# Optimization experiments

Hardware: AMD Instinct MI355X
Metric: run time of the kernel (lower is better)

Reference implementation:

```python
import jax, jax.numpy as jnp
import numpy as np

C = 64
CR = C // 8  # reduced channels for Q/K


def _conv1x1(x, W, b):
    # 1x1 conv == per-pixel linear over channels: x [b,c,h,w], W [o,c], b [o]
    return jnp.einsum('bchw,oc->bohw', x, W) + b[None, :, None, None]


def setup_inputs() -> dict:
    key = jax.random.key(0)
    ks = jax.random.split(key, 12)
    b, c, h, w = 8, C, 48, 48
    s = 1.0 / np.sqrt(c)
    inp = {
        'x1': jax.random.normal(ks[0], (b, c, h, w), jnp.float32),
        'x2': jax.random.normal(ks[1], (b, c, h, w), jnp.float32),
        'Wqk1': jax.random.normal(ks[2], (2 * CR, c), jnp.float32) * s,
        'bqk1': jnp.zeros((2 * CR,), jnp.float32),
        'Wqk2': jax.random.normal(ks[3], (2 * CR, c), jnp.float32) * s,
        'bqk2': jnp.zeros((2 * CR,), jnp.float32),
        'Wv1': jax.random.normal(ks[4], (c, c), jnp.float32) * s,
        'bv1': jnp.zeros((c,), jnp.float32),
        'Wv2': jax.random.normal(ks[5], (c, c), jnp.float32) * s,
        'bv2': jnp.zeros((c,), jnp.float32),
        'gamma': jnp.zeros((1,), jnp.float32) + 0.1,  # nonzero so output depends on attn
        'beta': jnp.zeros((1,), jnp.float32) + 0.1,
    }
    return inp


def reference(x1, x2, Wqk1, bqk1, Wqk2, bqk2, Wv1, bv1, Wv2, bv2, gamma, beta):
    b, c, h, w = x1.shape
    n = h * w
    qk1 = _conv1x1(x1, Wqk1, bqk1)
    qk2 = _conv1x1(x2, Wqk2, bqk2)
    q1, k1 = qk1[:, :CR], qk1[:, CR:]
    q2, k2 = qk2[:, :CR], qk2[:, CR:]
    # flatten spatial: [b, cr, n]
    q1 = q1.reshape(b, CR, n); k1 = k1.reshape(b, CR, n)
    q2 = q2.reshape(b, CR, n); k2 = k2.reshape(b, CR, n)
    v1 = _conv1x1(x1, Wv1, bv1).reshape(b, c, n)
    v2 = _conv1x1(x2, Wv2, bv2).reshape(b, c, n)
    # attn[b,i,j] = softmax_j( q[:, :, i] . k[:, :, j] )
    attn1 = jax.nn.softmax(jnp.einsum('bci,bcj->bij', q1, k1), axis=-1)
    attn2 = jax.nn.softmax(jnp.einsum('bci,bcj->bij', q2, k2), axis=-1)
    # out[:, :, j] = sum_i v[:, :, i] * attn[:, i, j]
    o1 = jnp.einsum('bci,bij->bcj', v1, attn2).reshape(b, c, h, w) * gamma + x1
    o2 = jnp.einsum('bci,bij->bcj', v2, attn1).reshape(b, c, h, w) * beta + x2
    return (o1, o2)
```

## Files before the change

### kernel.cpp

```cpp
#include <hip/hip_runtime.h>
#include <hip/hip_bf16.h>

#define NB   8
#define CCH  64
#define CR8  8
#define NPX  2304
#define BCN  (NB*CCH*NPX)
#define LOG2E 1.4426950408889634f

typedef short  short8   __attribute__((ext_vector_type(8)));
typedef unsigned short ushort8t __attribute__((ext_vector_type(8)));
typedef float  float4t  __attribute__((ext_vector_type(4)));
typedef float  float16t __attribute__((ext_vector_type(16)));

static __device__ __forceinline__ float fexp2(float x) {
    return __builtin_amdgcn_exp2f(x);
}
static __device__ __forceinline__ unsigned short bf16r(float f) {
    return (unsigned short)((__float_as_uint(f) + 0x8000u) >> 16);
}
static __device__ __forceinline__ unsigned int pack_bf16(float lo, float hi) {
    const unsigned int ul = __float_as_uint(lo) + 0x8000u;
    const unsigned int uh = __float_as_uint(hi) + 0x8000u;
    return __builtin_amdgcn_perm(uh, ul, 0x07060302u);
}
static __device__ __forceinline__ short8 pack8(const float* f) {
    union { unsigned int u[4]; short8 s; } r;
    #pragma unroll
    for (int j = 0; j < 4; j++) r.u[j] = pack_bf16(f[2*j], f[2*j+1]);
    return r.s;
}

#define WS_QB1 0
#define WS_KB1 (WS_QB1 + 147456)
#define WS_QB2 (WS_KB1 + 147456)
#define WS_KB2 (WS_QB2 + 147456)
#define WS_V1  (WS_KB2 + 147456)
#define WS_V2  (WS_V1 + BCN/2)
#define WS_PD  (WS_V2 + BCN/2)

__global__ __launch_bounds__(256) void proj_kernel(
    const float* __restrict__ x1, const float* __restrict__ x2,
    const float* __restrict__ Wqk1, const float* __restrict__ bqk1,
    const float* __restrict__ Wqk2, const float* __restrict__ bqk2,
    const float* __restrict__ Wv1,  const float* __restrict__ bv1,
    const float* __restrict__ Wv2,  const float* __restrict__ bv2,
    float* __restrict__ ws, float* __restrict__ out)
{
    const int t    = threadIdx.x;
    const int lane = t & 63;
    const int w    = t >> 6;
    const int n16  = lane & 15;
    const int c4   = lane >> 4;
    const int nt   = w & 1;
    const int mh   = w >> 1;
    const int b    = blockIdx.y;
    const int px   = blockIdx.x * 32 + nt * 16 + n16;

    const float* xsb[2];
    xsb[0] = x1 + ((size_t)b * CCH) * NPX + px;
    xsb[1] = x2 + ((size_t)b * CCH) * NPX + px;

    float xr[2][16];
    short8 bfrag[2][2];
    #pragma unroll
    for (int st = 0; st < 2; st++) {
        #pragma unroll
        for (int ch = 0; ch < 2; ch++) {
            #pragma unroll
            for (int j = 0; j < 8; j++)
                xr[st][ch * 8 + j] = xsb[st][(ch * 32 + c4 * 8 + j) * NPX];
            bfrag[st][ch] = pack8(&xr[st][ch * 8]);
        }
    }

    if (mh == 0) {
        #pragma unroll
        for (int st = 0; st < 2; st++) {
            float* outs = out + (st ? (size_t)BCN : 0);
            #pragma unroll
            for (int e = 0; e < 16; e++) {
                const int ch = (e >> 3) * 32 + c4 * 8 + (e & 7);
                outs[((size_t)b * CCH + ch) * NPX + px] = xr[st][e];
            }
        }
    }

    float4t acc[5];
    #pragma unroll
    for (int mt = 0; mt < 5; mt++) { acc[mt][0]=0.f; acc[mt][1]=0.f; acc[mt][2]=0.f; acc[mt][3]=0.f; }

    #pragma unroll
    for (int mt = 0; mt < 5; mt++) {
        const int mi  = mh * 5 + mt;
        const int isqk = (mi < 2);
        const int st  = isqk ? (mi & 1) : (mi >= 6);
        const float* Wb;
        int rowbase;
        if (isqk) { Wb = (mi == 0) ? Wqk1 : Wqk2; rowbase = 0; }
        else      { Wb = (mi >= 6) ? Wv2 : Wv1; rowbase = (mi - (mi >= 6 ? 6 : 2)) * 16; }
        const float* wrow = Wb + (size_t)(rowbase + n16) * 64 + c4 * 8;

        const short8 bf0 = st ? bfrag[1][0] : bfrag[0][0];
        const short8 bf1 = st ? bfrag[1][1] : bfrag[0][1];

        #pragma unroll
        for (int ch = 0; ch < 2; ch++) {
            float fa[8];
            const float4 a0 = *(const float4*)(wrow + ch * 32);
            const float4 a1 = *(const float4*)(wrow + ch * 32 + 4);
            fa[0] = a0.x; fa[1] = a0.y; fa[2] = a0.z; fa[3] = a0.w;
            fa[4] = a1.x; fa[5] = a1.y; fa[6] = a1.z; fa[7] = a1.w;
            acc[mt] = __builtin_amdgcn_mfma_f32_16x16x32_bf16(
                pack8(fa), ch ? bf1 : bf0, acc[mt], 0, 0, 0);
        }
    }

    #pragma unroll
    for (int mt = 0; mt < 5; mt++) {
        const int mi = mh * 5 + mt;
        if (mi < 2) {
            const int st = mi & 1;
            const float* bqk = st ? bqk2 : bqk1;
            unsigned short* qb = (unsigned short*)(ws + (st ? WS_QB2 : WS_QB1));
            unsigned short* kb = (unsigned short*)(ws + (st ? WS_KB2 : WS_KB1));
            const size_t rbase = (size_t)(b * NPX + px) * 16;
            #pragma unroll
            for (int r = 0; r < 4; r++) {
                const int oc = c4 * 4 + r;
                const float val = acc[mt][r] + bqk[oc];
                if (oc < 8)
                    qb[rbase + oc] = bf16r(val * LOG2E);
                else
                    kb[rbase + (oc - 8)] = bf16r(val);
            }
            ushort8t zq, zk;
            #pragma unroll
            for (int e = 0; e < 8; e++) { zq[e] = 0; zk[e] = 0; }
            zk[0] = 0x3F80; zk[1] = 0x3F80;
            if (c4 == 0) *(ushort8t*)(qb + rbase + 8) = zq;
            if (c4 == 2) *(ushort8t*)(kb + rbase + 8) = zk;
        } else {
            const int st = (mi >= 6);
            const int vt_ = mi - (st ? 6 : 2);
            const float* bv = st ? bv2 : bv1;
            unsigned short* v = (unsigned short*)(ws + (st ? WS_V2 : WS_V1));
            #pragma unroll
            for (int r = 0; r < 4; r++) {
                const int oc = vt_ * 16 + c4 * 4 + r;
                const float val = acc[mt][r] + bv[oc];
                v[((size_t)b * CCH + oc) * NPX + px] = bf16r(val);
            }
        }
    }
}

__global__ __launch_bounds__(256) void stats_kernel(float* __restrict__ ws)
{
    const int t  = threadIdx.x;
    const int w  = t >> 6;
    const int n  = t & 31;
    const int h  = (t & 63) >> 5;
    const int jsb = blockIdx.x;
    const int iq  = blockIdx.y;
    const int ab  = blockIdx.z;
    const int b   = ab & 7;
    const int a   = ab >> 3;

    const unsigned short* qb = (const unsigned short*)(ws + (a ? WS_QB2 : WS_QB1));
    const unsigned short* kb = (const unsigned short*)(ws + (a ? WS_KB2 : WS_KB1));
    float* pd = ws + WS_PD;

    __shared__ float red[4][288];

    const int j = jsb * 128 + w * 32 + n;
    const short8 kfrag = *(const short8*)(kb + (size_t)(b * NPX + j) * 16 + h * 8);

    const unsigned short* qp = qb + (size_t)(b * NPX + iq * 288 + n) * 16 + h * 8;
    short8 qf = *(const short8*)qp;

    for (int ib = 0; ib < 9; ib++) {
        qp += 512;
        short8 qn = qf;
        if (ib + 1 < 9) qn = *(const short8*)qp;
        float16t acc = {};
        acc = __builtin_amdgcn_mfma_f32_32x32x16_bf16(kfrag, qf, acc, 0, 0, 0);
        float s0 = 0.f, s1 = 0.f, s2 = 0.f, s3 = 0.f;
        #pragma unroll
        for (int r = 0; r < 4; r++) {
            s0 += fexp2(acc[4 * r + 0]);
            s1 += fexp2(acc[4 * r + 1]);
            s2 += fexp2(acc[4 * r + 2]);
            s3 += fexp2(acc[4 * r + 3]);
        }
        float ssum = (s0 + s1) + (s2 + s3);
        ssum += __shfl_xor(ssum, 32);
        if (h == 0) red[w][ib * 32 + n] = ssum;
        qf = qn;
    }
    __syncthreads();
    for (int idx = t; idx < 288; idx += 256)
        pd[((size_t)ab * 18 + jsb) * NPX + iq * 288 + idx] =
            red[0][idx] + red[1][idx] + red[2][idx] + red[3][idx];
}

__global__ __launch_bounds__(256) void merge_fold(float* __restrict__ ws)
{
    const float* pd = ws + WS_PD;
    const int t  = threadIdx.x;
    const int il = t & 63;
    const int pg = t >> 6;
    const int i  = blockIdx.x * 64 + il;
    const int ab = blockIdx.y;
    const int b  = ab & 7;
    const int a  = ab >> 3;

    __shared__ float red[4][64];

    const float* pb = pd + (size_t)ab * 18 * NPX + i;
    float d = 0.f;
    #pragma unroll
    for (int c = pg; c < 18; c += 4)
        d += pb[(size_t)c * NPX];
    red[pg][il] = d;
    __syncthreads();

    if (t < 64) {
        const float dt = (red[0][t] + red[1][t]) + (red[2][t] + red[3][t]);
        const float m = -__log2f(dt);
        const unsigned short mh = bf16r(m);
        __hip_bfloat16 hb; *(unsigned short*)&hb = mh;
        const unsigned short ml = bf16r(m - __bfloat162float(hb));
        unsigned short* qb = (unsigned short*)(ws + (a ? WS_QB2 : WS_QB1));
        const size_t rbase = (size_t)(b * NPX + blockIdx.x * 64 + t) * 16;
        qb[rbase + 8] = mh;
        qb[rbase + 9] = ml;
    }
}

__global__ __launch_bounds__(256) void out_kernel(
    const float* __restrict__ gamma, const float* __restrict__ beta,
    const float* __restrict__ ws, float* __restrict__ out)
{
    const int t  = threadIdx.x;
    const int jt = blockIdx.x;
    const int b  = blockIdx.y;
    const int z  = blockIdx.z;
    const int o  = z >> 2;
    const int ihalf = z & 3;

    const int a = o ? 0 : 1;
    const unsigned short* qb = (const unsigned short*)(ws + (a ? WS_QB2 : WS_QB1));
    const unsigned short* kb = (const unsigned short*)(ws + (a ? WS_KB2 : WS_KB1));
    const unsigned short* v  = (const unsigned short*)(ws + (o ? WS_V2 : WS_V1));
    const float  scale = o ? beta[0] : gamma[0];

    __shared__ unsigned short vt[64][72];
    __shared__ unsigned short pt[64][72];

    const int j0   = jt * 64;
    const int lane = t & 63;
    const int w    = t >> 6;
    const int n    = lane & 31;
    const int h    = lane >> 5;
    const int jh   = w & 1;
    const int ihq  = w >> 1;
    const int cbase = 32 * (w & 1);
    const int jbase = 32 * (w >> 1);

    const short8 kfrag = *(const short8*)(kb + (size_t)(b * NPX + j0 + 32 * jh + n) * 16 + h * 8);

    const int c0 = t >> 3, s80 = (t & 7) * 8;
    const int c1 = (t + 256) >> 3, s81 = ((t + 256) & 7) * 8;

    const int ibase = ihalf * 576;
    const unsigned short* vp0 = v + ((size_t)b * CCH + c0) * NPX + ibase + s80;
    const unsigned short* vp1 = v + ((size_t)b * CCH + c1) * NPX + ibase + s81;
    const unsigned short* qp  = qb + (size_t)(b * NPX + ibase + 32 * ihq + n) * 16 + h * 8;

    float4 vpre0 = *(const float4*)vp0;
    float4 vpre1 = *(const float4*)vp1;
    short8 qpre  = *(const short8*)qp;

    float16t oacc = {};

    for (int it = 0; it < 9; it++) {
        vp0 += 64; vp1 += 64; qp += 64 * 16;
        float4 vn0 = vpre0, vn1 = vpre1;
        short8 qn = qpre;
        if (it + 1 < 9) {
            vn0 = *(const float4*)vp0;
            vn1 = *(const float4*)vp1;
            qn  = *(const short8*)qp;
        }

        __syncthreads();

        *(float4*)&vt[c0][s80] = vpre0;
        *(float4*)&vt[c1][s81] = vpre1;

        float16t sc = {};
        sc = __builtin_amdgcn_mfma_f32_32x32x16_bf16(qpre, kfrag, sc, 0, 0, 0);

        #pragma unroll
        for (int gq = 0; gq < 4; gq++) {
            const int ibl = 32 * ihq + 8 * gq + 4 * h;
            uint2 pk;
            pk.x = pack_bf16(fexp2(sc[gq * 4 + 0]), fexp2(sc[gq * 4 + 1]));
            pk.y = pack_bf16(fexp2(sc[gq * 4 + 2]), fexp2(sc[gq * 4 + 3]));
            *(uint2*)&pt[32 * jh + n][ibl] = pk;
        }
        __syncthreads();

        #pragma unroll
        for (int kk = 0; kk < 4; kk++) {
            const short8 afrag = *(const short8*)&vt[cbase + n][kk * 16 + h * 8];
            const short8 bfrag = *(const short8*)&pt[jbase + n][kk * 16 + h * 8];
            oacc = __builtin_amdgcn_mfma_f32_32x32x16_bf16(afrag, bfrag, oacc, 0, 0, 0);
        }

        vpre0 = vn0; vpre1 = vn1; qpre = qn;
    }

    float* outp = out + (o ? BCN : 0) + (b * CCH + cbase) * NPX + j0 + jbase + n;
    #pragma unroll
    for (int r = 0; r < 16; r++) {
        const int row = (r & 3) + 8 * (r >> 2) + 4 * h;
        atomicAdd(outp + row * NPX, oacc[r] * scale);
    }
}

extern "C" void kernel_launch(void* const* d_in, const int* in_sizes, int n_in,
                              void* d_out, int out_size, void* d_ws, size_t ws_size,
                              hipStream_t stream)
{
    const float* x1   = (const float*)d_in[0];
    const float* x2   = (const float*)d_in[1];
    const float* Wqk1 = (const float*)d_in[2];
    const float* bqk1 = (const float*)d_in[3];
    const float* Wqk2 = (const float*)d_in[4];
    const float* bqk2 = (const float*)d_in[5];
    const float* Wv1  = (const float*)d_in[6];
    const float* bv1  = (const float*)d_in[7];
    const float* Wv2  = (const float*)d_in[8];
    const float* bv2  = (const float*)d_in[9];
    const float* gamma = (const float*)d_in[10];
    const float* beta  = (const float*)d_in[11];
    float* out = (float*)d_out;
    float* ws  = (float*)d_ws;

    proj_kernel<<<dim3(72, 8), 256, 0, stream>>>(
        x1, x2, Wqk1, bqk1, Wqk2, bqk2, Wv1, bv1, Wv2, bv2, ws, out);
    stats_kernel<<<dim3(18, 8, 16), 256, 0, stream>>>(ws);
    merge_fold<<<dim3(36, 16), 256, 0, stream>>>(ws);
    out_kernel<<<dim3(36, 8, 8), 256, 0, stream>>>(gamma, beta, ws, out);
}
```

Before: 145.0 us.

## Fuse softmax denominator merge into stats kernel via last-block atomic counter

Removes the separate merge_fold launch. Each stats block bumps a per-(ab,iq) atomic counter after writing its partial sums, and the last of the 18 column blocks reduces them, computes the log-sum and writes it into the Q buffer. The counters are zeroed by proj_kernel. This saves one kernel launch and its dependency gap, at the cost of a threadfence, an atomic per block, and a serial 18-way reduction done by one block per group.

```diff
diff --git a/kernel.cpp b/kernel.cpp
--- a/kernel.cpp
+++ b/kernel.cpp
@@ -38,6 +38,7 @@
 #define WS_V1  (WS_KB2 + 147456)
 #define WS_V2  (WS_V1 + BCN/2)
 #define WS_PD  (WS_V2 + BCN/2)
+#define WS_CNT (WS_PD + 2*NB*18*NPX)
 
 __global__ __launch_bounds__(256) void proj_kernel(
     const float* __restrict__ x1, const float* __restrict__ x2,
@@ -57,6 +58,9 @@
     const int b    = blockIdx.y;
     const int px   = blockIdx.x * 32 + nt * 16 + n16;
 
+    if (blockIdx.x == 0 && blockIdx.y == 0 && t < 128)
+        ((int*)(ws + WS_CNT))[t] = 0;
+
     const float* xsb[2];
     xsb[0] = x1 + ((size_t)b * CCH) * NPX + px;
     xsb[1] = x2 + ((size_t)b * CCH) * NPX + px;
@@ -170,8 +174,10 @@
     const unsigned short* qb = (const unsigned short*)(ws + (a ? WS_QB2 : WS_QB1));
     const unsigned short* kb = (const unsigned short*)(ws + (a ? WS_KB2 : WS_KB1));
     float* pd = ws + WS_PD;
+    int* cnt = (int*)(ws + WS_CNT);
 
     __shared__ float red[4][288];
+    __shared__ int lastflag;
 
     const int j = jsb * 128 + w * 32 + n;
     const short8 kfrag = *(const short8*)(kb + (size_t)(b * NPX + j) * 16 + h * 8);
@@ -202,39 +208,28 @@
     for (int idx = t; idx < 288; idx += 256)
         pd[((size_t)ab * 18 + jsb) * NPX + iq * 288 + idx] =
             red[0][idx] + red[1][idx] + red[2][idx] + red[3][idx];
-}
-
-__global__ __launch_bounds__(256) void merge_fold(float* __restrict__ ws)
-{
-    const float* pd = ws + WS_PD;
-    const int t  = threadIdx.x;
-    const int il = t & 63;
-    const int pg = t >> 6;
-    const int i  = blockIdx.x * 64 + il;
-    const int ab = blockIdx.y;
-    const int b  = ab & 7;
-    const int a  = ab >> 3;
-
-    __shared__ float red[4][64];
-
-    const float* pb = pd + (size_t)ab * 18 * NPX + i;
-    float d = 0.f;
-    #pragma unroll
-    for (int c = pg; c < 18; c += 4)
-        d += pb[(size_t)c * NPX];
-    red[pg][il] = d;
+
+    __threadfence();
+    if (t == 0)
+        lastflag = (atomicAdd(cnt + (ab * 8 + iq), 1) == 17);
     __syncthreads();
-
-    if (t < 64) {
-        const float dt = (red[0][t] + red[1][t]) + (red[2][t] + red[3][t]);
-        const float m = -__log2f(dt);
-        const unsigned short mh = bf16r(m);
-        __hip_bfloat16 hb; *(unsigned short*)&hb = mh;
-        const unsigned short ml = bf16r(m - __bfloat162float(hb));
-        unsigned short* qb = (unsigned short*)(ws + (a ? WS_QB2 : WS_QB1));
-        const size_t rbase = (size_t)(b * NPX + blockIdx.x * 64 + t) * 16;
-        qb[rbase + 8] = mh;
-        qb[rbase + 9] = ml;
+    if (lastflag) {
+        unsigned short* qbw = (unsigned short*)(ws + (a ? WS_QB2 : WS_QB1));
+        for (int ii = t; ii < 288; ii += 256) {
+            const int i = iq * 288 + ii;
+            const float* pb = pd + (size_t)ab * 18 * NPX + i;
+            float d = 0.f;
+            #pragma unroll
+            for (int c = 0; c < 18; c++)
+                d += pb[(size_t)c * NPX];
+            const float m = -__log2f(d);
+            const unsigned short mhi = bf16r(m);
+            __hip_bfloat16 hb; *(unsigned short*)&hb = mhi;
+            const unsigned short mlo = bf16r(m - __bfloat162float(hb));
+            const size_t rbase = (size_t)(b * NPX + i) * 16;
+            qbw[rbase + 8] = mhi;
+            qbw[rbase + 9] = mlo;
+        }
     }
 }
 
@@ -352,6 +347,5 @@
     proj_kernel<<<dim3(72, 8), 256, 0, stream>>>(
         x1, x2, Wqk1, bqk1, Wqk2, bqk2, Wv1, bv1, Wv2, bv2, ws, out);
     stats_kernel<<<dim3(18, 8, 16), 256, 0, stream>>>(ws);
-    merge_fold<<<dim3(36, 16), 256, 0, stream>>>(ws);
     out_kernel<<<dim3(36, 8, 8), 256, 0, stream>>>(gamma, beta, ws, out);
 }
```

Result: slower. 328.8 us (+126.7%).
